# Optimization experiments

Hardware: AMD Instinct MI355X
Metric: run time of the kernel (lower is better)

Reference implementation:

```python
import jax, jax.numpy as jnp
import numpy as np

# cfg constants (ProposalLayerSoft.__init__)
GRID_SIZE = jnp.array([8000.0, 8000.0, 2000.0], dtype=jnp.float32)   # MULTI_PERSON.SPACE_SIZE (mm)
CUBE_SIZE = jnp.array([128.0, 128.0, 64.0], dtype=jnp.float32)       # MULTI_PERSON.INITIAL_CUBE_SIZE
GRID_CENTER = jnp.array([0.0, 0.0, 300.0], dtype=jnp.float32)        # MULTI_PERSON.SPACE_CENTER
NUM_CAND = 10                                                         # MULTI_PERSON.MAX_PEOPLE_NUM
THRESHOLD = 0.3                                                       # MULTI_PERSON.THRESHOLD


def setup_inputs() -> dict:
    key = jax.random.key(0)
    # root heatmap cube in [0,1): [B, X, Y, Z]
    root_cubes = jax.random.uniform(key, (32, 128, 128, 64), dtype=jnp.float32)
    return {"root_cubes": root_cubes}


def _nms_topk(x):
    """3x3x3 max-pool peak suppression + top-k (repo's nms()).
    x: [B, X, Y, Z] -> (values [B,K], unravel_index [B,K,3] float)."""
    B, X, Y, Z = x.shape
    pooled = jax.lax.reduce_window(
        x, -jnp.inf, jax.lax.max,
        window_dimensions=(1, 3, 3, 3),
        window_strides=(1, 1, 1, 1),
        padding=[(0, 0), (1, 1), (1, 1), (1, 1)],
    )
    peaks = jnp.where(x == pooled, x, 0.0)           # keep only local maxima
    flat = peaks.reshape(B, X * Y * Z)
    topk_values, topk_index = jax.lax.top_k(flat, NUM_CAND)
    # C-order unravel (matches repo's get_index)
    ix = topk_index // (Y * Z)
    iy = (topk_index % (Y * Z)) // Z
    iz = topk_index % Z
    idx = jnp.stack([ix, iy, iz], axis=-1).astype(jnp.float32)  # [B, K, 3]
    return topk_values, idx


def reference(root_cubes):
    x = jax.lax.stop_gradient(root_cubes)  # original calls .detach()
    topk_values, topk_index = _nms_topk(x)
    # get_real_loc: voxel index -> world coords (mm)
    loc = topk_index / (CUBE_SIZE - 1.0) * GRID_SIZE + GRID_CENTER - GRID_SIZE / 2.0
    conf = (topk_values > THRESHOLD).astype(jnp.float32) - 1.0  # col 3
    grid_centers = jnp.concatenate(
        [loc, conf[..., None], topk_values[..., None]], axis=-1
    )  # [B, K, 5]: (x, y, z, valid_flag, score)
    return grid_centers
```

## Files before the change

### kernel.cpp

```cpp
#include <hip/hip_runtime.h>
#include <stdint.h>


#define TPB 256
#define NK 10
#define TY 10
#define BLOCKS_PER_B (4 * TY)
#define WCAP 512
#define THRV 0.999f
typedef unsigned long long u64;

__device__ __forceinline__ u64 bfly_max_u64(u64 v) {
#pragma unroll
  for (int off = 1; off < 64; off <<= 1) {
    u64 o = __shfl_xor(v, off, 64);
    v = (o > v) ? o : v;
  }
  return v;
}

__device__ __forceinline__ float dpp_nbr_a(float v) {
  return __int_as_float(__builtin_amdgcn_update_dpp(
      0, __float_as_int(v), 0x101, 0xF, 0xF, true));
}
__device__ __forceinline__ float dpp_nbr_b(float v) {
  return __int_as_float(__builtin_amdgcn_update_dpp(
      0, __float_as_int(v), 0x111, 0xF, 0xF, true));
}

template <bool PASS1>
__global__ __launch_bounds__(TPB, 5) void peaks_topk(
    const float* __restrict__ in, u64* __restrict__ part,
    unsigned* __restrict__ cnt) {
  __shared__ u64 cand[4][WCAP];
  __shared__ u64 wtop[4 * NK];
  __shared__ unsigned wcnts[4];
  const int b = blockIdx.z;
  if (!PASS1) {
    if (cnt[b] >= NK) return;
  }
  const int tid = threadIdx.x;
  const int w = tid >> 6, lane = tid & 63;
  const int yi = lane & 15, zq = lane >> 4;
  const int ty = blockIdx.x;
  const int seg = blockIdx.y * 2 + (w >> 1);
  const int zh = w & 1;
  const int y0 = ty * 14 - 1;
  const int gy = y0 + yi;
  const int cy = min(127, max(0, gy));
  const int x0 = seg << 4;
  const bool emit_ok = (yi >= 1) && (yi <= 14) && (gy <= 127);
  const int zoff = zh * 32 + (zq << 3);
  const int zlo = max(0, zoff - 1);
  const int zhi = min(63, zoff + 8);
  const bool lo_inf = (zq == 0) && (zh == 0);
  const bool hi_inf = (zq == 3) && (zh == 1);
  const float* __restrict__ py = in + ((size_t)b << 20) + ((size_t)cy << 6);

  int wcnt = 0;
  float vP[8], vC[8], vN[8];
  float loP, hiP, loC, hiC, loN, hiN;

  auto loadv = [&](int x, float* v, float& lo, float& hi) {
    const int cx = min(127, max(0, x));
    const float* p = py + ((size_t)cx << 13);
    float4 a = *(const float4*)(p + zoff);
    float4 bb = *(const float4*)(p + zoff + 4);
    v[0] = a.x;  v[1] = a.y;  v[2] = a.z;  v[3] = a.w;
    v[4] = bb.x; v[5] = bb.y; v[6] = bb.z; v[7] = bb.w;
    lo = p[zlo];
    hi = p[zhi];
  };

  loadv(x0 - 1, vP, loP, hiP);
  loadv(x0,     vC, loC, hiC);
  loadv(x0 + 1, vN, loN, hiN);

#pragma unroll 1
  for (int t = 0; t < 16; ++t) {
    const int x = x0 + t;
    bool anyc;
    if (PASS1) {
      float cm = fmaxf(fmaxf(fmaxf(vC[0], vC[1]), fmaxf(vC[2], vC[3])),
                       fmaxf(fmaxf(vC[4], vC[5]), fmaxf(vC[6], vC[7])));
      anyc = emit_ok && (cm > THRV);
    } else {
      anyc = emit_ok;
    }
    if (__ballot(anyc)) {
      float vlP = __shfl_up(vP[7], 16, 64), vrP = __shfl_down(vP[0], 16, 64);
      float vlC = __shfl_up(vC[7], 16, 64), vrC = __shfl_down(vC[0], 16, 64);
      float vlN = __shfl_up(vN[7], 16, 64), vrN = __shfl_down(vN[0], 16, 64);
      vlP = (zq == 0) ? (lo_inf ? -1e30f : loP) : vlP;
      vrP = (zq == 3) ? (hi_inf ? -1e30f : hiP) : vrP;
      vlC = (zq == 0) ? (lo_inf ? -1e30f : loC) : vlC;
      vrC = (zq == 3) ? (hi_inf ? -1e30f : hiC) : vrC;
      vlN = (zq == 0) ? (lo_inf ? -1e30f : loN) : vlN;
      vrN = (zq == 3) ? (hi_inf ? -1e30f : hiN) : vrN;
#pragma unroll
      for (int j = 0; j < 8; ++j) {
        const float v = vC[j];
        const bool pj = emit_ok && (PASS1 ? (v > THRV) : true);
        if (__ballot(pj)) {
          float aP = (j == 0) ? vlP : vP[j - 1];
          float cP = (j == 7) ? vrP : vP[j + 1];
          float aC = (j == 0) ? vlC : vC[j - 1];
          float cC = (j == 7) ? vrC : vC[j + 1];
          float aN = (j == 0) ? vlN : vN[j - 1];
          float cN = (j == 7) ? vrN : vN[j + 1];
          float zP = fmaxf(aP, fmaxf(vP[j], cP));
          float zC = fmaxf(aC, fmaxf(v, cC));
          float zN = fmaxf(aN, fmaxf(vN[j], cN));
          float xm = fmaxf(zP, fmaxf(zC, zN));
          float l = dpp_nbr_a(xm);
          float r = dpp_nbr_b(xm);
          float m27 = fmaxf(xm, fmaxf(l, r));
          const bool pred = pj && (v >= m27);
          u64 mask = __ballot(pred);
          if (pred) {
            unsigned g = ((unsigned)x << 13) | ((unsigned)gy << 6) |
                         (unsigned)(zoff + j);
            u64 key = ((u64)__float_as_uint(v) << 32) | (u64)(unsigned)(~g);
            int ofs = __builtin_amdgcn_mbcnt_hi(
                (unsigned)(mask >> 32),
                __builtin_amdgcn_mbcnt_lo((unsigned)mask, 0));
            int slot = wcnt + ofs;
            if (slot < WCAP) cand[w][slot] = key;
          }
          wcnt += (int)__popcll(mask);
        }
      }
    }
#pragma unroll
    for (int j = 0; j < 8; ++j) {
      vP[j] = vC[j];
      vC[j] = vN[j];
    }
    loP = loC; hiP = hiC; loC = loN; hiC = hiN;
    loadv(x + 2, vN, loN, hiN);
  }

  __builtin_amdgcn_s_waitcnt(0);
  const int count = min(wcnt, WCAP);
  u64 c[WCAP / 64];
#pragma unroll
  for (int i = 0; i < WCAP / 64; ++i) {
    int idx = lane + (i << 6);
    c[i] = (idx < count) ? cand[w][idx] : 0;
  }
  u64 mine = 0;
#pragma unroll 1
  for (int r = 0; r < NK; ++r) {
    u64 best = c[0];
#pragma unroll
    for (int i = 1; i < WCAP / 64; ++i) best = (c[i] > best) ? c[i] : best;
    u64 m = bfly_max_u64(best);
    if (m != 0 && best == m) {
#pragma unroll
      for (int i = 0; i < WCAP / 64; ++i)
        if (c[i] == m) c[i] = 0;
    }
    if (lane == r) mine = m;
  }
  if (lane < NK) wtop[w * NK + lane] = mine;
  if (lane == 0) wcnts[w] = (unsigned)wcnt;
  __syncthreads();

  if (w == 0) {
    u64 c0 = (lane < 4 * NK) ? wtop[lane] : 0;
    u64 mv = 0;
#pragma unroll 1
    for (int r = 0; r < NK; ++r) {
      u64 m = bfly_max_u64(c0);
      if (m != 0 && c0 == m) c0 = 0;
      if (lane == r) mv = m;
    }
    if (lane < NK) {
      const int bi = blockIdx.y * TY + ty;
      part[((size_t)b * BLOCKS_PER_B + bi) * NK + lane] = mv;
    }
    if (PASS1 && lane == 0) {
      unsigned s = wcnts[0] + wcnts[1] + wcnts[2] + wcnts[3];
      if (s) atomicAdd(&cnt[b], s);
    }
  }
}

__global__ __launch_bounds__(64) void final_select(
    const u64* __restrict__ part, float* __restrict__ out) {
  const int lane = threadIdx.x & 63;
  const int b = blockIdx.x;
  const int NKEY = BLOCKS_PER_B * NK;

  const u64* __restrict__ src = part + (size_t)b * NKEY;
  u64 c[7];
#pragma unroll
  for (int i = 0; i < 7; ++i) {
    int idx = lane + (i << 6);
    c[i] = (idx < NKEY) ? src[idx] : 0;
  }
  u64 mine = 0;
#pragma unroll 1
  for (int r = 0; r < NK; ++r) {
    u64 best = c[0];
#pragma unroll
    for (int i = 1; i < 7; ++i) best = (c[i] > best) ? c[i] : best;
    u64 m = bfly_max_u64(best);
    if (m != 0 && best == m) {
#pragma unroll
      for (int i = 0; i < 7; ++i)
        if (c[i] == m) c[i] = 0;
    }
    if (lane == r) mine = m;
  }
  if (lane < NK) {
    float val = 0.0f;
    unsigned g = 0u;
    if (mine != 0) {
      val = __uint_as_float((unsigned)(mine >> 32));
      g = ~((unsigned)mine);
    }
    float fx = (float)(g >> 13) * (8000.0f / 127.0f) - 4000.0f;
    float fy = (float)((g >> 6) & 127u) * (8000.0f / 127.0f) - 4000.0f;
    float fz = (float)(g & 63u) * (2000.0f / 63.0f) - 700.0f;
    float conf = (val > 0.3f) ? 0.0f : -1.0f;
    float* o = out + ((size_t)b * NK + lane) * 5;
    o[0] = fx; o[1] = fy; o[2] = fz; o[3] = conf; o[4] = val;
  }
}

extern "C" void kernel_launch(void* const* d_in, const int* in_sizes, int n_in,
                              void* d_out, int out_size, void* d_ws, size_t ws_size,
                              hipStream_t stream) {
  const float* in = (const float*)d_in[0];
  float* out = (float*)d_out;
  u64* part = (u64*)d_ws;
  const int B = in_sizes[0] >> 20;
  unsigned* cnt =
      (unsigned*)((char*)d_ws + (size_t)B * BLOCKS_PER_B * NK * sizeof(u64));

  hipMemsetAsync(cnt, 0, (size_t)B * sizeof(unsigned), stream);
  dim3 gridA(TY, 4, (unsigned)B);
  peaks_topk<true><<<gridA, dim3(TPB), 0, stream>>>(in, part, cnt);
  peaks_topk<false><<<gridA, dim3(TPB), 0, stream>>>(in, part, cnt);
  final_select<<<dim3((unsigned)B), dim3(64), 0, stream>>>(part, out);
}
```

Measured before the change: 223.7 us.

## Stream x-slabs through LDS ring with async global-to-LDS loads for pass one

Replaces the register-based first pass with a new kernel in which 512-thread blocks each stream a 16-plane x-slab through a 4-deep LDS ring. The ring is filled with global_load_lds using a swizzled layout, and waits on vmcnt let loads overlap with compute. The 27-neighbour max is done with LDS lookups, only for voxels above the threshold. The grid drops to 8 blocks per batch and the per-wave candidate buffer shrinks to 64 entries, with an overflow flag that sends the fallback dense pass to rerun. This aims to cut load overhead and redundant halo reads, at the cost of fewer blocks, so less parallelism and weaker latency hiding.

Result: slower. 287.5 us (+28.5%).

```diff
diff --git a/kernel.cpp b/kernel.cpp
--- a/kernel.cpp
+++ b/kernel.cpp
@@ -2,12 +2,16 @@
 #include <stdint.h>
 
 
+#define NK 10
+#define NSLAB 8
+#define SPB 512
+#define WCAP 64
+#define THRV 0.999f
 #define TPB 256
-#define NK 10
 #define TY 10
 #define BLOCKS_PER_B (4 * TY)
-#define WCAP 512
-#define THRV 0.999f
+#define FWCAP 512
+
 typedef unsigned long long u64;
 
 __device__ __forceinline__ u64 bfly_max_u64(u64 v) {
@@ -19,6 +23,172 @@
   return v;
 }
 
+__device__ __forceinline__ void load_lds16(const float* g, void* l) {
+  __builtin_amdgcn_global_load_lds(
+      (const __attribute__((address_space(1))) void*)g,
+      (__attribute__((address_space(3))) void*)l, 16, 0, 0);
+}
+
+__device__ __noinline__ float max27(const float* Pp, const float* Cp,
+                                    const float* Np, int y, int z) {
+  float m = -1e30f;
+#pragma unroll
+  for (int pp = 0; pp < 3; ++pp) {
+    const float* pl = (pp == 0) ? Pp : (pp == 1 ? Cp : Np);
+#pragma unroll
+    for (int dy = -1; dy <= 1; ++dy) {
+      int yy = y + dy;
+      if ((unsigned)yy > 127u) continue;
+      int yb = yy << 4, yx = yy & 7;
+#pragma unroll
+      for (int dz = -1; dz <= 1; ++dz) {
+        int zz = z + dz;
+        if ((unsigned)zz > 63u) continue;
+        int ch = yb + (((unsigned)zz >> 2) ^ yx);
+        m = fmaxf(m, pl[(ch << 2) + (zz & 3)]);
+      }
+    }
+  }
+  return m;
+}
+
+__global__ __launch_bounds__(SPB, 2) void peaks_stream(
+    const float* __restrict__ in, u64* __restrict__ part,
+    unsigned* __restrict__ cnt) {
+  __shared__ float ring[4][8192];
+  __shared__ u64 cand[8][WCAP];
+  __shared__ u64 wtop[8 * NK];
+  __shared__ unsigned wcnts[8];
+
+  const int tid = threadIdx.x;
+  const int w = tid >> 6, lane = tid & 63;
+  const int y = tid >> 2;
+  const int zq = tid & 3;
+  const int slab = blockIdx.x;
+  const int b = blockIdx.y;
+  const int x0 = slab << 4;
+  const float* __restrict__ bat = in + ((size_t)b << 20);
+
+  auto stage = [&](int xp, int s) {
+    const int cx = min(127, max(0, xp));
+    const float* src = bat + ((size_t)cx << 13);
+    float* dst = &ring[s][0];
+#pragma unroll
+    for (int i = 0; i < 4; ++i) {
+      int cbase = (w << 8) + (i << 6);
+      int ci = cbase + lane;
+      int cy2 = ci >> 4, k = ci & 15;
+      int kg = k ^ (cy2 & 7);
+      const float* sp = src + (((cy2 << 4) + kg) << 2);
+      load_lds16(sp, (void*)(dst + (cbase << 2)));
+    }
+  };
+
+  stage(x0 - 1, 0);
+  stage(x0,     1);
+  stage(x0 + 1, 2);
+  stage(x0 + 2, 3);
+
+  int wcnt = 0;
+  const int ybase = y << 4, yxr = y & 7;
+
+#pragma unroll 1
+  for (int t = 0; t < 16; ++t) {
+    if (t == 15) {
+      asm volatile("s_waitcnt vmcnt(0)" ::: "memory");
+    } else {
+      asm volatile("s_waitcnt vmcnt(4)" ::: "memory");
+    }
+    __builtin_amdgcn_s_barrier();
+    __builtin_amdgcn_sched_barrier(0);
+
+    const float* Pp = &ring[(t) & 3][0];
+    const float* Cp = &ring[(t + 1) & 3][0];
+    const float* Np = &ring[(t + 2) & 3][0];
+
+    float vC[16];
+#pragma unroll
+    for (int m = 0; m < 4; ++m) {
+      int ch = ybase + (((zq << 2) + m) ^ yxr);
+      const float4 q = *(const float4*)(Cp + (ch << 2));
+      vC[(m << 2) + 0] = q.x; vC[(m << 2) + 1] = q.y;
+      vC[(m << 2) + 2] = q.z; vC[(m << 2) + 3] = q.w;
+    }
+    float cmax = fmaxf(
+        fmaxf(fmaxf(fmaxf(vC[0], vC[1]), fmaxf(vC[2], vC[3])),
+              fmaxf(fmaxf(vC[4], vC[5]), fmaxf(vC[6], vC[7]))),
+        fmaxf(fmaxf(fmaxf(vC[8], vC[9]), fmaxf(vC[10], vC[11])),
+              fmaxf(fmaxf(vC[12], vC[13]), fmaxf(vC[14], vC[15]))));
+    if (__ballot(cmax > THRV)) {
+      const int x = x0 + t, zb = zq << 4;
+#pragma unroll
+      for (int j = 0; j < 16; ++j) {
+        const float v = vC[j];
+        const bool p1 = (v > THRV);
+        bool pred = false;
+        if (p1) pred = (v >= max27(Pp, Cp, Np, y, zb + j));
+        u64 mask = __ballot(pred);
+        if (pred) {
+          unsigned g = ((unsigned)x << 13) | ((unsigned)y << 6) |
+                       (unsigned)(zb + j);
+          u64 key = ((u64)__float_as_uint(v) << 32) | (u64)(unsigned)(~g);
+          int ofs = __builtin_amdgcn_mbcnt_hi(
+              (unsigned)(mask >> 32),
+              __builtin_amdgcn_mbcnt_lo((unsigned)mask, 0));
+          int slot = wcnt + ofs;
+          if (slot < WCAP) cand[w][slot] = key;
+        }
+        wcnt += (int)__popcll(mask);
+      }
+    }
+    __builtin_amdgcn_s_barrier();
+    __builtin_amdgcn_sched_barrier(0);
+    if (t <= 13) stage(x0 + t + 3, (t) & 3);
+  }
+
+  __builtin_amdgcn_s_waitcnt(0);
+  const int count = min(wcnt, WCAP);
+  u64 cc = (lane < count) ? cand[w][lane] : 0;
+  u64 mine = 0;
+#pragma unroll 1
+  for (int r = 0; r < NK; ++r) {
+    u64 m = bfly_max_u64(cc);
+    if (m != 0 && cc == m) cc = 0;
+    if (lane == r) mine = m;
+  }
+  if (lane < NK) wtop[w * NK + lane] = mine;
+  if (lane == 0) wcnts[w] = (unsigned)wcnt;
+  __syncthreads();
+
+  if (w == 0) {
+    u64 c0 = wtop[lane];
+    u64 c1 = (lane < 8 * NK - 64) ? wtop[64 + lane] : 0;
+    u64 mv = 0;
+#pragma unroll 1
+    for (int r = 0; r < NK; ++r) {
+      u64 best = (c0 > c1) ? c0 : c1;
+      u64 m = bfly_max_u64(best);
+      if (m != 0) {
+        if (c0 == m) c0 = 0;
+        else if (c1 == m) c1 = 0;
+      }
+      if (lane == r) mv = m;
+    }
+    if (lane < NK)
+      part[(size_t)b * 400 + slab * NK + lane] = mv;
+    if (lane == 0) {
+      unsigned s = wcnts[0] + wcnts[1] + wcnts[2] + wcnts[3] +
+                   wcnts[4] + wcnts[5] + wcnts[6] + wcnts[7];
+      if (s) atomicAdd(&cnt[b], s);
+      bool ovf = false;
+#pragma unroll
+      for (int i = 0; i < 8; ++i) ovf |= (wcnts[i] > WCAP);
+      if (ovf) atomicOr(&cnt[b], 0x80000000u);
+    }
+  }
+}
+
+
 __device__ __forceinline__ float dpp_nbr_a(float v) {
   return __int_as_float(__builtin_amdgcn_update_dpp(
       0, __float_as_int(v), 0x101, 0xF, 0xF, true));
@@ -28,16 +198,15 @@
       0, __float_as_int(v), 0x111, 0xF, 0xF, true));
 }
 
-template <bool PASS1>
-__global__ __launch_bounds__(TPB, 5) void peaks_topk(
+__global__ __launch_bounds__(TPB, 5) void peaks_fallback(
     const float* __restrict__ in, u64* __restrict__ part,
-    unsigned* __restrict__ cnt) {
-  __shared__ u64 cand[4][WCAP];
+    const unsigned* __restrict__ cnt) {
+  __shared__ u64 cand[4][FWCAP];
   __shared__ u64 wtop[4 * NK];
-  __shared__ unsigned wcnts[4];
   const int b = blockIdx.z;
-  if (!PASS1) {
-    if (cnt[b] >= NK) return;
+  {
+    unsigned cv = cnt[b];
+    if (cv < 0x80000000u && cv >= NK) return;
   }
   const int tid = threadIdx.x;
   const int w = tid >> 6, lane = tid & 63;
@@ -79,15 +248,7 @@
 #pragma unroll 1
   for (int t = 0; t < 16; ++t) {
     const int x = x0 + t;
-    bool anyc;
-    if (PASS1) {
-      float cm = fmaxf(fmaxf(fmaxf(vC[0], vC[1]), fmaxf(vC[2], vC[3])),
-                       fmaxf(fmaxf(vC[4], vC[5]), fmaxf(vC[6], vC[7])));
-      anyc = emit_ok && (cm > THRV);
-    } else {
-      anyc = emit_ok;
-    }
-    if (__ballot(anyc)) {
+    {
       float vlP = __shfl_up(vP[7], 16, 64), vrP = __shfl_down(vP[0], 16, 64);
       float vlC = __shfl_up(vC[7], 16, 64), vrC = __shfl_down(vC[0], 16, 64);
       float vlN = __shfl_up(vN[7], 16, 64), vrN = __shfl_down(vN[0], 16, 64);
@@ -99,36 +260,33 @@
       vrN = (zq == 3) ? (hi_inf ? -1e30f : hiN) : vrN;
 #pragma unroll
       for (int j = 0; j < 8; ++j) {
-        const float v = vC[j];
-        const bool pj = emit_ok && (PASS1 ? (v > THRV) : true);
-        if (__ballot(pj)) {
-          float aP = (j == 0) ? vlP : vP[j - 1];
-          float cP = (j == 7) ? vrP : vP[j + 1];
-          float aC = (j == 0) ? vlC : vC[j - 1];
-          float cC = (j == 7) ? vrC : vC[j + 1];
-          float aN = (j == 0) ? vlN : vN[j - 1];
-          float cN = (j == 7) ? vrN : vN[j + 1];
-          float zP = fmaxf(aP, fmaxf(vP[j], cP));
-          float zC = fmaxf(aC, fmaxf(v, cC));
-          float zN = fmaxf(aN, fmaxf(vN[j], cN));
-          float xm = fmaxf(zP, fmaxf(zC, zN));
-          float l = dpp_nbr_a(xm);
-          float r = dpp_nbr_b(xm);
-          float m27 = fmaxf(xm, fmaxf(l, r));
-          const bool pred = pj && (v >= m27);
-          u64 mask = __ballot(pred);
-          if (pred) {
-            unsigned g = ((unsigned)x << 13) | ((unsigned)gy << 6) |
-                         (unsigned)(zoff + j);
-            u64 key = ((u64)__float_as_uint(v) << 32) | (u64)(unsigned)(~g);
-            int ofs = __builtin_amdgcn_mbcnt_hi(
-                (unsigned)(mask >> 32),
-                __builtin_amdgcn_mbcnt_lo((unsigned)mask, 0));
-            int slot = wcnt + ofs;
-            if (slot < WCAP) cand[w][slot] = key;
-          }
-          wcnt += (int)__popcll(mask);
+        float aP = (j == 0) ? vlP : vP[j - 1];
+        float cP = (j == 7) ? vrP : vP[j + 1];
+        float aC = (j == 0) ? vlC : vC[j - 1];
+        float cC = (j == 7) ? vrC : vC[j + 1];
+        float aN = (j == 0) ? vlN : vN[j - 1];
+        float cN = (j == 7) ? vrN : vN[j + 1];
+        float v = vC[j];
+        float zP = fmaxf(aP, fmaxf(vP[j], cP));
+        float zC = fmaxf(aC, fmaxf(v, cC));
+        float zN = fmaxf(aN, fmaxf(vN[j], cN));
+        float xm = fmaxf(zP, fmaxf(zC, zN));
+        float l = dpp_nbr_a(xm);
+        float r = dpp_nbr_b(xm);
+        float m27 = fmaxf(xm, fmaxf(l, r));
+        const bool pred = emit_ok && (v >= m27);
+        u64 mask = __ballot(pred);
+        if (pred) {
+          unsigned g = ((unsigned)x << 13) | ((unsigned)gy << 6) |
+                       (unsigned)(zoff + j);
+          u64 key = ((u64)__float_as_uint(v) << 32) | (u64)(unsigned)(~g);
+          int ofs = __builtin_amdgcn_mbcnt_hi(
+              (unsigned)(mask >> 32),
+              __builtin_amdgcn_mbcnt_lo((unsigned)mask, 0));
+          int slot = wcnt + ofs;
+          if (slot < FWCAP) cand[w][slot] = key;
         }
+        wcnt += (int)__popcll(mask);
       }
     }
 #pragma unroll
@@ -141,10 +299,10 @@
   }
 
   __builtin_amdgcn_s_waitcnt(0);
-  const int count = min(wcnt, WCAP);
-  u64 c[WCAP / 64];
-#pragma unroll
-  for (int i = 0; i < WCAP / 64; ++i) {
+  const int count = min(wcnt, FWCAP);
+  u64 c[FWCAP / 64];
+#pragma unroll
+  for (int i = 0; i < FWCAP / 64; ++i) {
     int idx = lane + (i << 6);
     c[i] = (idx < count) ? cand[w][idx] : 0;
   }
@@ -153,17 +311,16 @@
   for (int r = 0; r < NK; ++r) {
     u64 best = c[0];
 #pragma unroll
-    for (int i = 1; i < WCAP / 64; ++i) best = (c[i] > best) ? c[i] : best;
+    for (int i = 1; i < FWCAP / 64; ++i) best = (c[i] > best) ? c[i] : best;
     u64 m = bfly_max_u64(best);
     if (m != 0 && best == m) {
 #pragma unroll
-      for (int i = 0; i < WCAP / 64; ++i)
+      for (int i = 0; i < FWCAP / 64; ++i)
         if (c[i] == m) c[i] = 0;
     }
     if (lane == r) mine = m;
   }
   if (lane < NK) wtop[w * NK + lane] = mine;
-  if (lane == 0) wcnts[w] = (unsigned)wcnt;
   __syncthreads();
 
   if (w == 0) {
@@ -177,27 +334,31 @@
     }
     if (lane < NK) {
       const int bi = blockIdx.y * TY + ty;
-      part[((size_t)b * BLOCKS_PER_B + bi) * NK + lane] = mv;
-    }
-    if (PASS1 && lane == 0) {
-      unsigned s = wcnts[0] + wcnts[1] + wcnts[2] + wcnts[3];
-      if (s) atomicAdd(&cnt[b], s);
+      part[(size_t)b * 400 + bi * NK + lane] = mv;
     }
   }
 }
 
 __global__ __launch_bounds__(64) void final_select(
-    const u64* __restrict__ part, float* __restrict__ out) {
+    const u64* __restrict__ part, const unsigned* __restrict__ cnt,
+    float* __restrict__ out) {
   const int lane = threadIdx.x & 63;
   const int b = blockIdx.x;
-  const int NKEY = BLOCKS_PER_B * NK;
-
-  const u64* __restrict__ src = part + (size_t)b * NKEY;
+  const u64* __restrict__ src = part + (size_t)b * 400;
+  unsigned cv = cnt[b];
+  const bool dense = !(cv < 0x80000000u && cv >= NK);
   u64 c[7];
-#pragma unroll
-  for (int i = 0; i < 7; ++i) {
-    int idx = lane + (i << 6);
-    c[i] = (idx < NKEY) ? src[idx] : 0;
+  if (dense) {
+#pragma unroll
+    for (int i = 0; i < 7; ++i) {
+      int idx = lane + (i << 6);
+      c[i] = (idx < 400) ? src[idx] : 0;
+    }
+  } else {
+    c[0] = src[lane];
+    c[1] = (lane < 8 * NK - 64) ? src[64 + lane] : 0;
+#pragma unroll
+    for (int i = 2; i < 7; ++i) c[i] = 0;
   }
   u64 mine = 0;
 #pragma unroll 1
@@ -237,11 +398,12 @@
   u64* part = (u64*)d_ws;
   const int B = in_sizes[0] >> 20;
   unsigned* cnt =
-      (unsigned*)((char*)d_ws + (size_t)B * BLOCKS_PER_B * NK * sizeof(u64));
+      (unsigned*)((char*)d_ws + (size_t)B * 400 * sizeof(u64));
 
   hipMemsetAsync(cnt, 0, (size_t)B * sizeof(unsigned), stream);
-  dim3 gridA(TY, 4, (unsigned)B);
-  peaks_topk<true><<<gridA, dim3(TPB), 0, stream>>>(in, part, cnt);
-  peaks_topk<false><<<gridA, dim3(TPB), 0, stream>>>(in, part, cnt);
-  final_select<<<dim3((unsigned)B), dim3(64), 0, stream>>>(part, out);
-}
+  peaks_stream<<<dim3(NSLAB, (unsigned)B), dim3(SPB), 0, stream>>>(in, part,
+                                                                   cnt);
+  peaks_fallback<<<dim3(TY, 4, (unsigned)B), dim3(TPB), 0, stream>>>(in, part,
+                                                                     cnt);
+  final_select<<<dim3((unsigned)B), dim3(64), 0, stream>>>(part, cnt, out);
+}
```
